# Optimization experiments

Hardware: AMD Instinct MI355X
Metric: run time of the kernel (lower is better)

Reference implementation:

```python
import jax, jax.numpy as jnp
import numpy as np
import math

D_MODEL = 1024
N_HEADS = 16
HEAD_DIM = D_MODEL // N_HEADS
B, S = 2, 2048


def setup_inputs() -> dict:
    key = jax.random.key(0)
    ks = jax.random.split(key, 12)
    sd = 1.0 / math.sqrt(D_MODEL)
    inp = {
        "x": jax.random.normal(ks[0], (B, S, D_MODEL), dtype=jnp.float32),
        "time_gaps": jax.random.uniform(ks[1], (B, S, 1), dtype=jnp.float32),
        "mask": jnp.ones((B, S), dtype=jnp.int32),
        "Wq": jax.random.normal(ks[2], (D_MODEL, D_MODEL), dtype=jnp.float32) * sd,
        "bq": jnp.zeros((D_MODEL,), dtype=jnp.float32),
        "Wk": jax.random.normal(ks[3], (D_MODEL, D_MODEL), dtype=jnp.float32) * sd,
        "bk": jnp.zeros((D_MODEL,), dtype=jnp.float32),
        "Wv": jax.random.normal(ks[4], (D_MODEL, D_MODEL), dtype=jnp.float32) * sd,
        "bv": jnp.zeros((D_MODEL,), dtype=jnp.float32),
        "Wo": jax.random.normal(ks[5], (D_MODEL, D_MODEL), dtype=jnp.float32) * sd,
        "bo": jnp.zeros((D_MODEL,), dtype=jnp.float32),
        "Wt": jax.random.normal(ks[6], (D_MODEL, 1), dtype=jnp.float32),
        "bt": jnp.zeros((D_MODEL,), dtype=jnp.float32),
    }
    return inp


def reference(x, time_gaps, mask, Wq, bq, Wk, bk, Wv, bv, Wo, bo, Wt, bt):
    Bb, Ss, _ = x.shape
    # time embedding: Linear(1, d_model)
    time_emb = time_gaps @ Wt.T + bt            # [B,S,D]
    x_time = x + time_emb

    def split_heads(t):
        return t.reshape(Bb, Ss, N_HEADS, HEAD_DIM).transpose(0, 2, 1, 3)  # [B,H,S,d]

    q = split_heads(x_time @ Wq.T + bq)
    k = split_heads(x_time @ Wk.T + bk)
    v = split_heads(x @ Wv.T + bv)

    scores = jnp.einsum('bhqd,bhkd->bhqk', q, k) / math.sqrt(HEAD_DIM)
    # padding mask: mask==0 positions set to -1e9 (mask broadcast as [B,1,1,S])
    pad = (mask == 0)[:, None, None, :]
    scores = jnp.where(pad, -1e9, scores)
    # causal mask
    causal = jnp.triu(jnp.ones((Ss, Ss), dtype=bool), k=1)
    scores = jnp.where(causal, -1e9, scores)

    attn = jax.nn.softmax(scores, axis=-1)      # dropout is identity in eval
    out = jnp.einsum('bhqk,bhkd->bhqd', attn, v)
    out = out.transpose(0, 2, 1, 3).reshape(Bb, Ss, D_MODEL)
    return out @ Wo.T + bo
```

## Files before the change

### kernel.cpp

```cpp
#include <hip/hip_runtime.h>

typedef short v8s __attribute__((ext_vector_type(8)));
typedef short v4s __attribute__((ext_vector_type(4)));
typedef float v4f __attribute__((ext_vector_type(4)));
typedef int   v4i __attribute__((ext_vector_type(4)));

constexpr int Bb = 2, S = 2048, D = 1024, H = 16;
constexpr int M = Bb * S;

#define DEV __device__ __forceinline__

DEV short f2bf(float f){
  unsigned u = __builtin_bit_cast(unsigned, f);
  u = (u + 0x7FFF + ((u >> 16) & 1)) >> 16;
  return (short)u;
}

DEV int swz(int r){ return (r ^ (r >> 2)) & 7; }

DEV int cvtpk(float lo, float hi){
  int r;
  asm("v_cvt_pk_bf16_f32 %0, %1, %2" : "=v"(r) : "v"(lo), "v"(hi));
  return r;
}

DEV float max3f(float a, float b, float c){
  float r;
  asm("v_max3_f32 %0, %1, %2, %3" : "=v"(r) : "v"(a), "v"(b), "v"(c));
  return r;
}

#define EXP2 exp2f

#define GLDS(gp, lp) __builtin_amdgcn_global_load_lds( \
    (const __attribute__((address_space(1))) void*)(gp), \
    (__attribute__((address_space(3))) void*)(lp), 16, 0, 0)

struct PrepArgs {
  const float* x; const float* tg; const float* Wt; const float* bt;
  const float* Ws0; const float* Ws1; const float* Ws2; const float* Ws3;
  short* Wd0; short* Wd1; short* Wd2; short* Wd3;
  short* xb; short* xtb;
};
__global__ void prep_all(PrepArgs a){
  const int bx = blockIdx.x;
  if (bx < 4096){
    int i = bx * 256 + threadIdx.x;
    int row = i >> 8;
    int c4  = i & 255;
    float4 xv = reinterpret_cast<const float4*>(a.x)[i];
    float4 wv = reinterpret_cast<const float4*>(a.Wt)[c4];
    float4 bv = reinterpret_cast<const float4*>(a.bt)[c4];
    float g = a.tg[row];
    float xs[4] = {xv.x, xv.y, xv.z, xv.w};
    float ws[4] = {wv.x, wv.y, wv.z, wv.w};
    float bs[4] = {bv.x, bv.y, bv.z, bv.w};
    v4s p, q;
    #pragma unroll
    for (int e = 0; e < 4; ++e){
      p[e] = f2bf(xs[e]);
      q[e] = f2bf(xs[e] + g * ws[e] + bs[e]);
    }
    *reinterpret_cast<v4s*>(&a.xb[(size_t)i * 4])  = p;
    *reinterpret_cast<v4s*>(&a.xtb[(size_t)i * 4]) = q;
  } else {
    const int bi = bx - 4096;
    const int widx = bi >> 10;
    const float* src = widx == 0 ? a.Ws0 : widx == 1 ? a.Ws1 : widx == 2 ? a.Ws2 : a.Ws3;
    short* dst = widx == 0 ? a.Wd0 : widx == 1 ? a.Wd1 : widx == 2 ? a.Wd2 : a.Wd3;
    int i = (bi & 1023) * 256 + threadIdx.x;
    float4 v = reinterpret_cast<const float4*>(src)[i];
    v4s o; o[0] = f2bf(v.x); o[1] = f2bf(v.y); o[2] = f2bf(v.z); o[3] = f2bf(v.w);
    *reinterpret_cast<v4s*>(&dst[(size_t)i * 4]) = o;
  }
}

template<int MODE>
DEV void gemm_core(short* lds,
                   const short* __restrict__ A, const short* __restrict__ Bw,
                   const float* __restrict__ bias, float alpha, void* __restrict__ Cout,
                   int ldc, int m0, int n0){
  short* As = lds;
  short* Bs = lds + 2 * 128 * 64;
  const int t = threadIdx.x;
  const int w = t >> 6, l = t & 63;
  const int wm = (w >> 1) * 64, wn = (w & 1) * 64;

  v4f acc[4][4] = {};

  auto stage = [&](int kt, int buf){
    const int k0 = kt * 64;
    #pragma unroll
    for (int j = 0; j < 4; ++j){
      const int cix = j * 256 + t;
      const int row = cix >> 3;
      const int c   = (cix & 7) ^ swz(row);
      GLDS(A  + (size_t)(m0 + row) * D + k0 + c * 8, As + buf * 8192 + cix * 8);
      GLDS(Bw + (size_t)(n0 + row) * D + k0 + c * 8, Bs + buf * 8192 + cix * 8);
    }
  };

  stage(0, 0);
  for (int kt = 0; kt < 16; ++kt){
    const int cur = kt & 1;
    __syncthreads();
    if (kt < 15) stage(kt + 1, cur ^ 1);
    #pragma unroll
    for (int kk = 0; kk < 2; ++kk){
      v8s af[4], bfr[4];
      #pragma unroll
      for (int mi = 0; mi < 4; ++mi){
        const int R = wm + mi * 16 + (l & 15);
        af[mi] = *reinterpret_cast<const v8s*>(&As[cur * 8192 + R * 64 + (((kk * 4 + (l >> 4)) ^ swz(R)) * 8)]);
      }
      #pragma unroll
      for (int ni = 0; ni < 4; ++ni){
        const int R = wn + ni * 16 + (l & 15);
        bfr[ni] = *reinterpret_cast<const v8s*>(&Bs[cur * 8192 + R * 64 + (((kk * 4 + (l >> 4)) ^ swz(R)) * 8)]);
      }
      __builtin_amdgcn_s_setprio(1);
      #pragma unroll
      for (int mi = 0; mi < 4; ++mi)
        #pragma unroll
        for (int ni = 0; ni < 4; ++ni)
          acc[mi][ni] = __builtin_amdgcn_mfma_f32_16x16x32_bf16(af[mi], bfr[ni], acc[mi][ni], 0, 0, 0);
      __builtin_amdgcn_s_setprio(0);
    }
  }

  #pragma unroll
  for (int mi = 0; mi < 4; ++mi){
    const int row = m0 + wm + mi * 16 + (l >> 4) * 4;
    #pragma unroll
    for (int ni = 0; ni < 4; ++ni){
      const int col = n0 + wn + ni * 16 + (l & 15);
      const float bcol = (MODE == 1) ? 0.f : bias[col];
      #pragma unroll
      for (int r = 0; r < 4; ++r){
        float bsel = (MODE == 1) ? bias[row + r] : bcol;
        float val = (acc[mi][ni][r] + bsel) * alpha;
        if (MODE == 2) reinterpret_cast<float*>(Cout)[(size_t)(row + r) * ldc + col] = val;
        else           reinterpret_cast<short*>(Cout)[(size_t)(row + r) * ldc + col] = f2bf(val);
      }
    }
  }
}

template<int MODE>
__global__ __launch_bounds__(256, 2)
void gemm_bt(const short* __restrict__ A, const short* __restrict__ Bw,
             const float* __restrict__ bias, float alpha, void* __restrict__ Cout, int ldc){
  __shared__ short lds[4 * 128 * 64];
  gemm_core<MODE>(lds, A, Bw, bias, alpha, Cout, ldc, blockIdx.x * 128, blockIdx.y * 128);
}

__global__ __launch_bounds__(256, 2)
void gemm_qkv(const short* __restrict__ xtb, const short* __restrict__ xb,
              const short* __restrict__ Wqb, const short* __restrict__ Wkb,
              const short* __restrict__ Wvb,
              const float* __restrict__ bq, const float* __restrict__ bk,
              const float* __restrict__ bv, float qalpha,
              short* __restrict__ Qb, short* __restrict__ Kb, short* __restrict__ VTb){
  __shared__ short lds[4 * 128 * 64];
  const int id = blockIdx.x;
  if (id < 512){
    const int li = id;
    const int yq = li >> 5;
    const bool isK = yq >= 8;
    gemm_core<0>(lds, xtb, isK ? Wkb : Wqb, isK ? bk : bq, isK ? 1.0f : qalpha,
                 isK ? (void*)Kb : (void*)Qb, D, (li & 31) * 128, (yq & 7) * 128);
  } else {
    const int li = id - 512;
    gemm_core<1>(lds, Wvb, xb, bv, 1.0f, VTb, M, (li & 7) * 128, (li >> 3) * 128);
  }
}

__global__ __launch_bounds__(256, 4)
void attn_kernel(const short* __restrict__ Q, const short* __restrict__ K,
                 const short* __restrict__ VT, const int* __restrict__ maskp,
                 short* __restrict__ O){
  __shared__ short Ks[2][64 * 64];
  __shared__ short Vs[2][64 * 64];
  __shared__ int mflag;
  const int t = threadIdx.x, w = t >> 6, l = t & 63;
  const int g = l >> 4, q16 = l & 15;
  const int bh = blockIdx.x, b = bh >> 4, h = bh & 15;
  const int yy = (int)blockIdx.y;
  const int qx = (yy < 8) ? 31 - yy : (yy < 16) ? yy - 8 : (yy < 24) ? 39 - yy : yy - 16;
  const int q0 = qx * 64;
  const int qw = q0 + w * 16;
  const int qg = qw + q16;
  const int nkt = qx + 1;

  if (t == 0) mflag = 1;
  __syncthreads();
  {
    bool ok = true;
    const int tot = nkt * 64;
    for (int i = t * 4; i < tot; i += 1024){
      v4i mm = *reinterpret_cast<const v4i*>(&maskp[b * S + i]);
      ok = ok && (mm[0] != 0) && (mm[1] != 0) && (mm[2] != 0) && (mm[3] != 0);
    }
    if (!__all(ok)) mflag = 0;
  }
  __syncthreads();
  const bool ALLV = (mflag != 0);

  v8s qf[2];
  #pragma unroll
  for (int kc = 0; kc < 2; ++kc)
    qf[kc] = *reinterpret_cast<const v8s*>(
        &Q[(size_t)(b * S + qg) * D + h * 64 + kc * 32 + g * 8]);

  int kOff[4][2], vOff[4][2];
  #pragma unroll
  for (int nt = 0; nt < 4; ++nt){
    const int R = 32 * (nt >> 1) + 8 * (q16 >> 2) + 4 * (nt & 1) + (l & 3);
    #pragma unroll
    for (int kc = 0; kc < 2; ++kc)
      kOff[nt][kc] = R * 64 + (((kc * 4 + g) ^ swz(R)) * 8);
  }
  #pragma unroll
  for (int dt = 0; dt < 4; ++dt){
    const int R = dt * 16 + q16;
    #pragma unroll
    for (int kc = 0; kc < 2; ++kc)
      vOff[dt][kc] = R * 64 + (((kc * 4 + g) ^ swz(R)) * 8);
  }

  v4f accOT[4] = {};
  v4f accL = {};
  float mrow = -1e30f;

  const v4i onesW = {0x3F803F80, 0x3F803F80, 0x3F803F80, 0x3F803F80};
  const v8s onesv = __builtin_bit_cast(v8s, onesW);

  auto stage = [&](int kt){
    const int buf = kt & 1;
    const int kv0 = kt * 64;
    #pragma unroll
    for (int j = 0; j < 2; ++j){
      const int cix = j * 256 + t;
      const int row = cix >> 3;
      const int c   = (cix & 7) ^ swz(row);
      GLDS(K  + (size_t)(b * S + kv0 + row) * D + h * 64 + c * 8, &Ks[buf][cix * 8]);
      GLDS(VT + (size_t)(h * 64 + row) * M + b * S + kv0 + c * 8, &Vs[buf][cix * 8]);
    }
  };

  auto softmax_pv = [&](float (&p)[16], const short* vb){
    float t0 = max3f(p[0], p[1], p[2]);
    float t1 = max3f(p[3], p[4], p[5]);
    float t2 = max3f(p[6], p[7], p[8]);
    float t3 = max3f(p[9], p[10], p[11]);
    float t4 = max3f(p[12], p[13], p[14]);
    float tm = max3f(max3f(t0, t1, t2), t3, fmaxf(t4, p[15]));
    if (!__all(tm <= mrow + 8.0f)){
      float tmax = fmaxf(tm, __shfl_xor(tm, 16));
      tmax = fmaxf(tmax, __shfl_xor(tmax, 32));
      const float mnew = fmaxf(mrow, tmax);
      const float resc = EXP2(mrow - mnew);
      #pragma unroll
      for (int dt = 0; dt < 4; ++dt) accOT[dt] *= resc;
      accL *= resc;
      mrow = mnew;
    }
    #pragma unroll
    for (int j = 0; j < 16; ++j) p[j] = EXP2(p[j] - mrow);

    int pb[2][4];
    #pragma unroll
    for (int kc = 0; kc < 2; ++kc)
      #pragma unroll
      for (int s = 0; s < 4; ++s){
        const int base = (2 * kc + (s >> 1)) * 4 + (s & 1) * 2;
        pb[kc][s] = cvtpk(p[base], p[base + 1]);
      }

    __builtin_amdgcn_s_setprio(1);
    #pragma unroll
    for (int kc = 0; kc < 2; ++kc){
      v4i tmp = {pb[kc][0], pb[kc][1], pb[kc][2], pb[kc][3]};
      v8s pbv = __builtin_bit_cast(v8s, tmp);
      accL = __builtin_amdgcn_mfma_f32_16x16x32_bf16(onesv, pbv, accL, 0, 0, 0);
      #pragma unroll
      for (int dt = 0; dt < 4; ++dt){
        v8s vf = *reinterpret_cast<const v8s*>(vb + vOff[dt][kc]);
        accOT[dt] = __builtin_amdgcn_mfma_f32_16x16x32_bf16(vf, pbv, accOT[dt], 0, 0, 0);
      }
    }
    __builtin_amdgcn_s_setprio(0);
  };

  auto qk = [&](const short* kb, v4f (&sc)[4]){
    __builtin_amdgcn_s_setprio(1);
    #pragma unroll
    for (int nt = 0; nt < 4; ++nt)
      #pragma unroll
      for (int kc = 0; kc < 2; ++kc){
        v8s kf = *reinterpret_cast<const v8s*>(kb + kOff[nt][kc]);
        sc[nt] = __builtin_amdgcn_mfma_f32_16x16x32_bf16(kf, qf[kc], sc[nt], 0, 0, 0);
      }
    __builtin_amdgcn_s_setprio(0);
  };

  stage(0);

  if (ALLV){
    for (int kt = 0; kt < nkt; ++kt){
      asm volatile("s_waitcnt vmcnt(0)" ::: "memory");
      __builtin_amdgcn_s_barrier();
      if (kt + 1 < nkt) stage(kt + 1);

      const short* kb = Ks[kt & 1];
      const short* vb = Vs[kt & 1];

      v4f sc[4] = {};
      qk(kb, sc);

      float p[16];
      if (kt < qx){
        #pragma unroll
        for (int j = 0; j < 16; ++j) p[j] = sc[j >> 2][j & 3];
      } else {
        const int kv0 = kt * 64;
        #pragma unroll
        for (int nt = 0; nt < 4; ++nt)
          #pragma unroll
          for (int r = 0; r < 4; ++r){
            const int kvg = kv0 + 32 * (nt >> 1) + 8 * g + 4 * (nt & 1) + r;
            p[nt * 4 + r] = (kvg > qg) ? -1e30f : sc[nt][r];
          }
      }
      softmax_pv(p, vb);
    }
  } else {
    for (int kt = 0; kt < nkt; ++kt){
      asm volatile("s_waitcnt vmcnt(0)" ::: "memory");
      __builtin_amdgcn_s_barrier();
      if (kt + 1 < nkt) stage(kt + 1);

      const short* kb = Ks[kt & 1];
      const short* vb = Vs[kt & 1];
      const int kv0 = kt * 64;

      v4i mq[4];
      #pragma unroll
      for (int nt = 0; nt < 4; ++nt)
        mq[nt] = *reinterpret_cast<const v4i*>(
            &maskp[b * S + kv0 + 32 * (nt >> 1) + 8 * g + 4 * (nt & 1)]);

      v4f sc[4] = {};
      qk(kb, sc);

      float p[16];
      #pragma unroll
      for (int nt = 0; nt < 4; ++nt)
        #pragma unroll
        for (int r = 0; r < 4; ++r){
          const int kvg = kv0 + 32 * (nt >> 1) + 8 * g + 4 * (nt & 1) + r;
          const int kvx = (mq[nt][r] != 0) ? kvg : 0x7fffffff;
          p[nt * 4 + r] = (kvx > qg) ? -1e30f : sc[nt][r];
        }
      softmax_pv(p, vb);
    }
  }

  const float inv = 1.0f / accL[0];
  #pragma unroll
  for (int dt = 0; dt < 4; ++dt){
    v4s o4;
    #pragma unroll
    for (int r = 0; r < 4; ++r) o4[r] = f2bf(accOT[dt][r] * inv);
    *reinterpret_cast<v4s*>(
        &O[(size_t)(b * S + qg) * D + h * 64 + dt * 16 + g * 4]) = o4;
  }
}

extern "C" void kernel_launch(void* const* d_in, const int* in_sizes, int n_in,
                              void* d_out, int out_size, void* d_ws, size_t ws_size,
                              hipStream_t stream){
  const float* x   = (const float*)d_in[0];
  const float* tg  = (const float*)d_in[1];
  const int*   msk = (const int*)d_in[2];
  const float* Wq  = (const float*)d_in[3];
  const float* bq  = (const float*)d_in[4];
  const float* Wk  = (const float*)d_in[5];
  const float* bk  = (const float*)d_in[6];
  const float* Wv  = (const float*)d_in[7];
  const float* bv  = (const float*)d_in[8];
  const float* Wo  = (const float*)d_in[9];
  const float* bo  = (const float*)d_in[10];
  const float* Wt  = (const float*)d_in[11];
  const float* bt  = (const float*)d_in[12];

  char* ws = (char*)d_ws;
  const size_t MB = 1u << 20;
  short* xb  = (short*)(ws);
  short* xtb = (short*)(ws + 8 * MB);
  short* Wqb = (short*)(ws + 16 * MB);
  short* Wkb = (short*)(ws + 18 * MB);
  short* Wvb = (short*)(ws + 20 * MB);
  short* Wob = (short*)(ws + 22 * MB);
  short* Qb  = (short*)(ws + 24 * MB);
  short* Kb  = (short*)(ws + 32 * MB);
  short* VTb = (short*)(ws + 40 * MB);
  short* Ab  = (short*)(ws + 48 * MB);

  PrepArgs pa;
  pa.x = x; pa.tg = tg; pa.Wt = Wt; pa.bt = bt;
  pa.Ws0 = Wq; pa.Ws1 = Wk; pa.Ws2 = Wv; pa.Ws3 = Wo;
  pa.Wd0 = Wqb; pa.Wd1 = Wkb; pa.Wd2 = Wvb; pa.Wd3 = Wob;
  pa.xb = xb; pa.xtb = xtb;
  prep_all<<<8192, 256, 0, stream>>>(pa);

  const float qalpha = 0.125f * 1.4426950408889634f;
  gemm_qkv<<<768, 256, 0, stream>>>(xtb, xb, Wqb, Wkb, Wvb, bq, bk, bv, qalpha,
                                    Qb, Kb, VTb);

  attn_kernel<<<dim3(Bb * H, 32), 256, 0, stream>>>(Qb, Kb, VTb, msk, Ab);

  gemm_bt<2><<<dim3(M / 128, D / 128), 256, 0, stream>>>(Ab, Wob, bo, 1.0f, (float*)d_out, D);
}
```

Baseline: 103.8 us.

## Double attention query tile to 128 rows, two 16-row slices per wave

The attention kernel now gives each block 128 query rows instead of 64, and each wave handles two 16-row slices that share every K/V fragment read from LDS. This halves K/V staging traffic per query and doubles MFMA work per LDS load. Waves skip KV tiles that lie fully above their causal diagonal. The cost is more registers (launch bounds relaxed to 2 blocks per SIMD), half as many blocks in the grid, and wave imbalance on diagonal tiles.

New measurement: 115.2 us. 1.11x slower.

```diff
diff --git a/kernel.cpp b/kernel.cpp
--- a/kernel.cpp
+++ b/kernel.cpp
@@ -175,7 +175,7 @@
   }
 }
 
-__global__ __launch_bounds__(256, 4)
+__global__ __launch_bounds__(256, 2)
 void attn_kernel(const short* __restrict__ Q, const short* __restrict__ K,
                  const short* __restrict__ VT, const int* __restrict__ maskp,
                  short* __restrict__ O){
@@ -186,11 +186,10 @@
   const int g = l >> 4, q16 = l & 15;
   const int bh = blockIdx.x, b = bh >> 4, h = bh & 15;
   const int yy = (int)blockIdx.y;
-  const int qx = (yy < 8) ? 31 - yy : (yy < 16) ? yy - 8 : (yy < 24) ? 39 - yy : yy - 16;
-  const int q0 = qx * 64;
-  const int qw = q0 + w * 16;
-  const int qg = qw + q16;
-  const int nkt = qx + 1;
+  const int qx = (yy < 8) ? 15 - yy : yy - 8;
+  const int q0 = qx * 128;
+  const int qw = q0 + w * 32;
+  const int nkt = 2 * qx + 2;
 
   if (t == 0) mflag = 1;
   __syncthreads();
@@ -206,11 +205,13 @@
   __syncthreads();
   const bool ALLV = (mflag != 0);
 
-  v8s qf[2];
+  v8s qf[2][2];
   #pragma unroll
-  for (int kc = 0; kc < 2; ++kc)
-    qf[kc] = *reinterpret_cast<const v8s*>(
-        &Q[(size_t)(b * S + qg) * D + h * 64 + kc * 32 + g * 8]);
+  for (int mi = 0; mi < 2; ++mi)
+    #pragma unroll
+    for (int kc = 0; kc < 2; ++kc)
+      qf[mi][kc] = *reinterpret_cast<const v8s*>(
+          &Q[(size_t)(b * S + qw + mi * 16 + q16) * D + h * 64 + kc * 32 + g * 8]);
 
   int kOff[4][2], vOff[4][2];
   #pragma unroll
@@ -228,9 +229,9 @@
       vOff[dt][kc] = R * 64 + (((kc * 4 + g) ^ swz(R)) * 8);
   }
 
-  v4f accOT[4] = {};
-  v4f accL = {};
-  float mrow = -1e30f;
+  v4f accOT[2][4] = {};
+  v4f accL[2] = {};
+  float mrow[2] = {-1e30f, -1e30f};
 
   const v4i onesW = {0x3F803F80, 0x3F803F80, 0x3F803F80, 0x3F803F80};
   const v8s onesv = __builtin_bit_cast(v8s, onesW);
@@ -248,27 +249,38 @@
     }
   };
 
-  auto softmax_pv = [&](float (&p)[16], const short* vb){
+  auto qk2 = [&](const short* kb, v4f (&sc)[2][4]){
+    __builtin_amdgcn_s_setprio(1);
+    #pragma unroll
+    for (int nt = 0; nt < 4; ++nt)
+      #pragma unroll
+      for (int kc = 0; kc < 2; ++kc){
+        v8s kf = *reinterpret_cast<const v8s*>(kb + kOff[nt][kc]);
+        sc[0][nt] = __builtin_amdgcn_mfma_f32_16x16x32_bf16(kf, qf[0][kc], sc[0][nt], 0, 0, 0);
+        sc[1][nt] = __builtin_amdgcn_mfma_f32_16x16x32_bf16(kf, qf[1][kc], sc[1][nt], 0, 0, 0);
+      }
+    __builtin_amdgcn_s_setprio(0);
+  };
+
+  auto softmax_pack = [&](float (&p)[16], int mi, int (&pb)[2][4]){
     float t0 = max3f(p[0], p[1], p[2]);
     float t1 = max3f(p[3], p[4], p[5]);
     float t2 = max3f(p[6], p[7], p[8]);
     float t3 = max3f(p[9], p[10], p[11]);
     float t4 = max3f(p[12], p[13], p[14]);
     float tm = max3f(max3f(t0, t1, t2), t3, fmaxf(t4, p[15]));
-    if (!__all(tm <= mrow + 8.0f)){
+    if (!__all(tm <= mrow[mi] + 8.0f)){
       float tmax = fmaxf(tm, __shfl_xor(tm, 16));
       tmax = fmaxf(tmax, __shfl_xor(tmax, 32));
-      const float mnew = fmaxf(mrow, tmax);
-      const float resc = EXP2(mrow - mnew);
-      #pragma unroll
-      for (int dt = 0; dt < 4; ++dt) accOT[dt] *= resc;
-      accL *= resc;
-      mrow = mnew;
-    }
-    #pragma unroll
-    for (int j = 0; j < 16; ++j) p[j] = EXP2(p[j] - mrow);
-
-    int pb[2][4];
+      const float mnew = fmaxf(mrow[mi], tmax);
+      const float resc = EXP2(mrow[mi] - mnew);
+      #pragma unroll
+      for (int dt = 0; dt < 4; ++dt) accOT[mi][dt] *= resc;
+      accL[mi] *= resc;
+      mrow[mi] = mnew;
+    }
+    #pragma unroll
+    for (int j = 0; j < 16; ++j) p[j] = EXP2(p[j] - mrow[mi]);
     #pragma unroll
     for (int kc = 0; kc < 2; ++kc)
       #pragma unroll
@@ -276,31 +288,25 @@
         const int base = (2 * kc + (s >> 1)) * 4 + (s & 1) * 2;
         pb[kc][s] = cvtpk(p[base], p[base + 1]);
       }
-
+  };
+
+  auto pv2 = [&](const short* vb, int (&pb0)[2][4], int (&pb1)[2][4]){
     __builtin_amdgcn_s_setprio(1);
     #pragma unroll
     for (int kc = 0; kc < 2; ++kc){
-      v4i tmp = {pb[kc][0], pb[kc][1], pb[kc][2], pb[kc][3]};
-      v8s pbv = __builtin_bit_cast(v8s, tmp);
-      accL = __builtin_amdgcn_mfma_f32_16x16x32_bf16(onesv, pbv, accL, 0, 0, 0);
+      v4i t0 = {pb0[kc][0], pb0[kc][1], pb0[kc][2], pb0[kc][3]};
+      v4i t1 = {pb1[kc][0], pb1[kc][1], pb1[kc][2], pb1[kc][3]};
+      v8s pv0 = __builtin_bit_cast(v8s, t0);
+      v8s pv1 = __builtin_bit_cast(v8s, t1);
+      accL[0] = __builtin_amdgcn_mfma_f32_16x16x32_bf16(onesv, pv0, accL[0], 0, 0, 0);
+      accL[1] = __builtin_amdgcn_mfma_f32_16x16x32_bf16(onesv, pv1, accL[1], 0, 0, 0);
       #pragma unroll
       for (int dt = 0; dt < 4; ++dt){
         v8s vf = *reinterpret_cast<const v8s*>(vb + vOff[dt][kc]);
-        accOT[dt] = __builtin_amdgcn_mfma_f32_16x16x32_bf16(vf, pbv, accOT[dt], 0, 0, 0);
-      }
-    }
-    __builtin_amdgcn_s_setprio(0);
-  };
-
-  auto qk = [&](const short* kb, v4f (&sc)[4]){
-    __builtin_amdgcn_s_setprio(1);
-    #pragma unroll
-    for (int nt = 0; nt < 4; ++nt)
-      #pragma unroll
-      for (int kc = 0; kc < 2; ++kc){
-        v8s kf = *reinterpret_cast<const v8s*>(kb + kOff[nt][kc]);
-        sc[nt] = __builtin_amdgcn_mfma_f32_16x16x32_bf16(kf, qf[kc], sc[nt], 0, 0, 0);
-      }
+        accOT[0][dt] = __builtin_amdgcn_mfma_f32_16x16x32_bf16(vf, pv0, accOT[0][dt], 0, 0, 0);
+        accOT[1][dt] = __builtin_amdgcn_mfma_f32_16x16x32_bf16(vf, pv1, accOT[1][dt], 0, 0, 0);
+      }
+    }
     __builtin_amdgcn_s_setprio(0);
   };
 
@@ -312,68 +318,92 @@
       __builtin_amdgcn_s_barrier();
       if (kt + 1 < nkt) stage(kt + 1);
 
+      const int kv0 = kt * 64;
+      if (kv0 > qw + 31) continue;
+
       const short* kb = Ks[kt & 1];
       const short* vb = Vs[kt & 1];
 
-      v4f sc[4] = {};
-      qk(kb, sc);
-
-      float p[16];
-      if (kt < qx){
+      v4f sc[2][4] = {};
+      qk2(kb, sc);
+
+      int pb0[2][4], pb1[2][4];
+      if (kv0 + 63 <= qw){
         #pragma unroll
-        for (int j = 0; j < 16; ++j) p[j] = sc[j >> 2][j & 3];
+        for (int mi = 0; mi < 2; ++mi){
+          float p[16];
+          #pragma unroll
+          for (int j = 0; j < 16; ++j) p[j] = sc[mi][j >> 2][j & 3];
+          softmax_pack(p, mi, mi == 0 ? pb0 : pb1);
+        }
       } else {
-        const int kv0 = kt * 64;
+        #pragma unroll
+        for (int mi = 0; mi < 2; ++mi){
+          const int qg = qw + mi * 16 + q16;
+          float p[16];
+          #pragma unroll
+          for (int nt = 0; nt < 4; ++nt)
+            #pragma unroll
+            for (int r = 0; r < 4; ++r){
+              const int kvg = kv0 + 32 * (nt >> 1) + 8 * g + 4 * (nt & 1) + r;
+              p[nt * 4 + r] = (kvg > qg) ? -1e30f : sc[mi][nt][r];
+            }
+          softmax_pack(p, mi, mi == 0 ? pb0 : pb1);
+        }
+      }
+      pv2(vb, pb0, pb1);
+    }
+  } else {
+    for (int kt = 0; kt < nkt; ++kt){
+      asm volatile("s_waitcnt vmcnt(0)" ::: "memory");
+      __builtin_amdgcn_s_barrier();
+      if (kt + 1 < nkt) stage(kt + 1);
+
+      const int kv0 = kt * 64;
+      if (kv0 > qw + 31) continue;
+
+      const short* kb = Ks[kt & 1];
+      const short* vb = Vs[kt & 1];
+
+      v4i mq[4];
+      #pragma unroll
+      for (int nt = 0; nt < 4; ++nt)
+        mq[nt] = *reinterpret_cast<const v4i*>(
+            &maskp[b * S + kv0 + 32 * (nt >> 1) + 8 * g + 4 * (nt & 1)]);
+
+      v4f sc[2][4] = {};
+      qk2(kb, sc);
+
+      int pb0[2][4], pb1[2][4];
+      #pragma unroll
+      for (int mi = 0; mi < 2; ++mi){
+        const int qg = qw + mi * 16 + q16;
+        float p[16];
         #pragma unroll
         for (int nt = 0; nt < 4; ++nt)
           #pragma unroll
           for (int r = 0; r < 4; ++r){
             const int kvg = kv0 + 32 * (nt >> 1) + 8 * g + 4 * (nt & 1) + r;
-            p[nt * 4 + r] = (kvg > qg) ? -1e30f : sc[nt][r];
+            const int kvx = (mq[nt][r] != 0) ? kvg : 0x7fffffff;
+            p[nt * 4 + r] = (kvx > qg) ? -1e30f : sc[mi][nt][r];
           }
-      }
-      softmax_pv(p, vb);
-    }
-  } else {
-    for (int kt = 0; kt < nkt; ++kt){
-      asm volatile("s_waitcnt vmcnt(0)" ::: "memory");
-      __builtin_amdgcn_s_barrier();
-      if (kt + 1 < nkt) stage(kt + 1);
-
-      const short* kb = Ks[kt & 1];
-      const short* vb = Vs[kt & 1];
-      const int kv0 = kt * 64;
-
-      v4i mq[4];
-      #pragma unroll
-      for (int nt = 0; nt < 4; ++nt)
-        mq[nt] = *reinterpret_cast<const v4i*>(
-            &maskp[b * S + kv0 + 32 * (nt >> 1) + 8 * g + 4 * (nt & 1)]);
-
-      v4f sc[4] = {};
-      qk(kb, sc);
-
-      float p[16];
-      #pragma unroll
-      for (int nt = 0; nt < 4; ++nt)
-        #pragma unroll
-        for (int r = 0; r < 4; ++r){
-          const int kvg = kv0 + 32 * (nt >> 1) + 8 * g + 4 * (nt & 1) + r;
-          const int kvx = (mq[nt][r] != 0) ? kvg : 0x7fffffff;
-          p[nt * 4 + r] = (kvx > qg) ? -1e30f : sc[nt][r];
-        }
-      softmax_pv(p, vb);
-    }
-  }
-
-  const float inv = 1.0f / accL[0];
+        softmax_pack(p, mi, mi == 0 ? pb0 : pb1);
+      }
+      pv2(vb, pb0, pb1);
+    }
+  }
+
   #pragma unroll
-  for (int dt = 0; dt < 4; ++dt){
-    v4s o4;
-    #pragma unroll
-    for (int r = 0; r < 4; ++r) o4[r] = f2bf(accOT[dt][r] * inv);
-    *reinterpret_cast<v4s*>(
-        &O[(size_t)(b * S + qg) * D + h * 64 + dt * 16 + g * 4]) = o4;
+  for (int mi = 0; mi < 2; ++mi){
+    const float inv = 1.0f / accL[mi][0];
+    #pragma unroll
+    for (int dt = 0; dt < 4; ++dt){
+      v4s o4;
+      #pragma unroll
+      for (int r = 0; r < 4; ++r) o4[r] = f2bf(accOT[mi][dt][r] * inv);
+      *reinterpret_cast<v4s*>(
+          &O[(size_t)(b * S + qw + mi * 16 + q16) * D + h * 64 + dt * 16 + g * 4]) = o4;
+    }
   }
 }
 
@@ -418,7 +448,7 @@
   gemm_qkv<<<768, 256, 0, stream>>>(xtb, xb, Wqb, Wkb, Wvb, bq, bk, bv, qalpha,
                                     Qb, Kb, VTb);
 
-  attn_kernel<<<dim3(Bb * H, 32), 256, 0, stream>>>(Qb, Kb, VTb, msk, Ab);
+  attn_kernel<<<dim3(Bb * H, 16), 256, 0, stream>>>(Qb, Kb, VTb, msk, Ab);
 
   gemm_bt<2><<<dim3(M / 128, D / 128), 256, 0, stream>>>(Ab, Wob, bo, 1.0f, (float*)d_out, D);
 }
```
